# Kernel tuning notes

Measured on AMD Instinct MI355X. Metric: run time of the kernel, lower is better.

Reference implementation:

```python
import jax, jax.numpy as jnp
import numpy as np

B, N, L = 1, 2048, 256
DX, DY, H = 1536, 768, 12
D = DX // H  # head_dim = 128
EPS_MOD = 1e-6   # modulated_rmsnorm eps
EPS_QK = 1e-5    # per-head RMSNorm eps


def setup_inputs() -> dict:
    key = jax.random.key(0)
    ks = jax.random.split(key, 16)
    def n(k, shape, s=1.0):
        return jax.random.normal(k, shape, dtype=jnp.float32) * s
    # rotary tables: (N, H, D//2), shared across heads
    pos = jnp.arange(N, dtype=jnp.float32)
    inv_freq = 1.0 / (10000.0 ** (jnp.arange(D // 2, dtype=jnp.float32) / (D // 2)))
    ang = pos[:, None] * inv_freq[None, :]                       # (N, D/2)
    rope_cos = jnp.broadcast_to(jnp.cos(ang)[:, None, :], (N, H, D // 2))
    rope_sin = jnp.broadcast_to(jnp.sin(ang)[:, None, :], (N, H, D // 2))
    return {
        "x": n(ks[0], (B, N, DX)),
        "y": n(ks[1], (B, L, DY)),
        "scale_x": n(ks[2], (B, DX), 0.1),
        "scale_y": n(ks[3], (B, DY), 0.1),
        "rope_cos": rope_cos,
        "rope_sin": rope_sin,
        "Wqkv_x": n(ks[4], (DX, 3 * DX), 0.02),
        "bqkv_x": jnp.zeros((3 * DX,), jnp.float32),
        "Wqkv_y": n(ks[5], (DY, 3 * DX), 0.02),
        "bqkv_y": jnp.zeros((3 * DX,), jnp.float32),
        "q_norm_x_w": jnp.ones((D,), jnp.float32),
        "k_norm_x_w": jnp.ones((D,), jnp.float32),
        "q_norm_y_w": jnp.ones((D,), jnp.float32),
        "k_norm_y_w": jnp.ones((D,), jnp.float32),
        "Wproj_x": n(ks[6], (DX, DX), 0.02),
        "bproj_x": jnp.zeros((DX,), jnp.float32),
        "Wproj_y": n(ks[7], (DX, DY), 0.02),
        "bproj_y": jnp.zeros((DY,), jnp.float32),
    }


def _rms(v, eps):
    return v * jax.lax.rsqrt(jnp.mean(v * v, axis=-1, keepdims=True) + eps)


def _rope(q, cos, sin):
    # q: (B, S, H, D); cos/sin: (S, H, D/2); even/odd interleaved rotation
    qe, qo = q[..., 0::2], q[..., 1::2]
    re = qe * cos - qo * sin
    ro = qe * sin + qo * cos
    return jnp.stack([re, ro], axis=-1).reshape(q.shape)


def reference(x, y, scale_x, scale_y, rope_cos, rope_sin,
              Wqkv_x, bqkv_x, Wqkv_y, bqkv_y,
              q_norm_x_w, k_norm_x_w, q_norm_y_w, k_norm_y_w,
              Wproj_x, bproj_x, Wproj_y, bproj_y):
    b, n, dx = x.shape
    _, l, _ = y.shape
    h, d = H, D
    # --- visual stream ---
    xm = _rms(x, EPS_MOD) * (1.0 + scale_x[:, None, :])          # modulated_rmsnorm
    qkv = (xm @ Wqkv_x + bqkv_x).reshape(b, n, 3, h, d)
    q_x, k_x, v_x = qkv[:, :, 0], qkv[:, :, 1], qkv[:, :, 2]
    q_x = _rope(_rms(q_x, EPS_QK) * q_norm_x_w, rope_cos, rope_sin)
    k_x = _rope(_rms(k_x, EPS_QK) * k_norm_x_w, rope_cos, rope_sin)
    # --- text stream ---
    ym = _rms(y, EPS_MOD) * (1.0 + scale_y[:, None, :])
    qkvy = (ym @ Wqkv_y + bqkv_y).reshape(b, l, 3, h, d)
    q_y, k_y, v_y = qkvy[:, :, 0], qkvy[:, :, 1], qkvy[:, :, 2]
    q_y = _rms(q_y, EPS_QK) * q_norm_y_w
    k_y = _rms(k_y, EPS_QK) * k_norm_y_w
    # --- joint attention over concatenated sequence (B, H, N+L, D) ---
    q = jnp.concatenate([q_x, q_y], axis=1).transpose(0, 2, 1, 3)
    k = jnp.concatenate([k_x, k_y], axis=1).transpose(0, 2, 1, 3)
    v = jnp.concatenate([v_x, v_y], axis=1).transpose(0, 2, 1, 3)
    scale = 1.0 / np.sqrt(d).astype(np.float32)
    attn = jax.nn.softmax(jnp.einsum('bhqd,bhkd->bhqk', q, k) * scale, axis=-1)
    out = jnp.einsum('bhqk,bhkd->bhqd', attn, v)
    out = out.transpose(0, 2, 1, 3).reshape(b, n + l, h * d)
    x_out = out[:, :n] @ Wproj_x + bproj_x
    y_out = out[:, n:] @ Wproj_y + bproj_y
    return (x_out, y_out)
```

## Files before the change

### kernel.cpp

```cpp
#include <hip/hip_runtime.h>

typedef unsigned short u16;
typedef __attribute__((ext_vector_type(8))) short short8;
typedef __attribute__((ext_vector_type(4))) short short4v;
typedef __attribute__((ext_vector_type(4))) float floatx4;

__device__ __forceinline__ u16 f2bf(float f) {
  return (u16)((__float_as_uint(f) + 0x8000u) >> 16);
}
__device__ __forceinline__ float bf2f(u16 v) {
  return __uint_as_float(((unsigned)v) << 16);
}
__device__ __forceinline__ unsigned pack_bf2(float a, float b) {
  const unsigned ua = __float_as_uint(a) + 0x8000u;
  const unsigned ub = __float_as_uint(b) + 0x8000u;
  return __builtin_amdgcn_perm(ub, ua, 0x07060302);
}

#define GLD16(g, l) __builtin_amdgcn_global_load_lds( \
    (const __attribute__((address_space(1))) void*)(g), \
    (__attribute__((address_space(3))) void*)(l), 16, 0, 0)

__global__ __launch_bounds__(256) void prep(const float* __restrict__ W0, u16* __restrict__ T0,
                                            const float* __restrict__ W1, u16* __restrict__ T1,
                                            const float* __restrict__ W2, u16* __restrict__ T2,
                                            const float* __restrict__ W3, u16* __restrict__ T3,
                                            const float* __restrict__ x, const float* __restrict__ scale_x,
                                            const float* __restrict__ y, const float* __restrict__ scale_y,
                                            u16* __restrict__ xm, u16* __restrict__ ym) {
  __shared__ float t[32][33];
  const int z = blockIdx.z;
  if (z < 4) {
    const float* in; u16* out; int K, N;
    switch (z) {
      case 0: in = W0; out = T0; K = 1536; N = 4608; break;
      case 1: in = W1; out = T1; K = 768;  N = 4608; break;
      case 2: in = W2; out = T2; K = 1536; N = 1536; break;
      default: in = W3; out = T3; K = 1536; N = 768; break;
    }
    const int n0 = blockIdx.x * 32, k0 = blockIdx.y * 32;
    if (n0 >= N || k0 >= K) return;
    const int tx = threadIdx.x, ty = threadIdx.y;
#pragma unroll
    for (int i = 0; i < 32; i += 8)
      t[ty + i][tx] = in[(size_t)(k0 + ty + i) * N + n0 + tx];
    __syncthreads();
#pragma unroll
    for (int i = 0; i < 32; i += 8)
      out[(size_t)(n0 + ty + i) * K + k0 + tx] = f2bf(t[tx][ty + i]);
  } else {
    const int row = blockIdx.y * 144 + blockIdx.x;
    if (row >= 2304) return;
    const int tid = threadIdx.y * 32 + threadIdx.x;
    const float* xr; const float* sc; u16* dst; int D;
    if (row < 2048) { D = 1536; xr = x + (size_t)row * D; sc = scale_x; dst = xm + (size_t)row * D; }
    else { D = 768; xr = y + (size_t)(row - 2048) * D; sc = scale_y; dst = ym + (size_t)(row - 2048) * D; }
    float ss = 0.f;
    for (int c = tid; c < D; c += 256) { float v = xr[c]; ss += v * v; }
    for (int off = 32; off > 0; off >>= 1) ss += __shfl_down(ss, off);
    __shared__ float red[4];
    if ((tid & 63) == 0) red[tid >> 6] = ss;
    __syncthreads();
    const float tot = red[0] + red[1] + red[2] + red[3];
    const float r = rsqrtf(tot / (float)D + 1e-6f);
    for (int c = tid; c < D; c += 256)
      dst[c] = f2bf(xr[c] * r * (1.0f + sc[c]));
  }
}

template <bool BOUT>
__global__ __launch_bounds__(256) void gemm2(const u16* __restrict__ A0, const u16* __restrict__ BT0,
                                             const float* __restrict__ bias0, void* __restrict__ C0,
                                             int M0, int N0, int K0,
                                             const u16* __restrict__ A1, const u16* __restrict__ BT1,
                                             const float* __restrict__ bias1, void* __restrict__ C1,
                                             int M1, int N1, int K1) {
  const u16 *A, *BT; const float* bias; void* Cout; int M, N, K;
  if (blockIdx.z == 0) { A = A0; BT = BT0; bias = bias0; Cout = C0; M = M0; N = N0; K = K0; }
  else { A = A1; BT = BT1; bias = bias1; Cout = C1; M = M1; N = N1; K = K1; }
  const int bm = blockIdx.y * 128, bn = blockIdx.x * 128;
  if (bm >= M || bn >= N) return;

  __shared__ __align__(16) u16 As[128 * 32];
  __shared__ __align__(16) u16 Bs[128 * 32];
  const int tid = threadIdx.x;
  const int lane = tid & 63, wave = tid >> 6;
  const int wm = (wave & 1) * 64, wn = (wave >> 1) * 64;
  const int row16 = lane & 15, quad = lane >> 4;

  floatx4 acc[4][4] = {};
  const int r0 = lane >> 2, c4 = (lane & 3) * 8;
  const u16* Ag0 = A + (size_t)(bm + wave * 16 + r0) * K + c4;
  const u16* Ag1 = A + (size_t)(bm + (wave + 4) * 16 + r0) * K + c4;
  const u16* Bg0 = BT + (size_t)(bn + wave * 16 + r0) * K + c4;
  const u16* Bg1 = BT + (size_t)(bn + (wave + 4) * 16 + r0) * K + c4;
  u16* As0 = As + wave * 512; u16* As1 = As + (wave + 4) * 512;
  u16* Bs0 = Bs + wave * 512; u16* Bs1 = Bs + (wave + 4) * 512;

  for (int k0 = 0; k0 < K; k0 += 32) {
    GLD16(Ag0 + k0, As0);
    GLD16(Ag1 + k0, As1);
    GLD16(Bg0 + k0, Bs0);
    GLD16(Bg1 + k0, Bs1);
    __syncthreads();
    short8 af[4], bf[4];
#pragma unroll
    for (int i = 0; i < 4; i++) {
      af[i] = *(const short8*)&As[(wm + i * 16 + row16) * 32 + quad * 8];
      bf[i] = *(const short8*)&Bs[(wn + i * 16 + row16) * 32 + quad * 8];
    }
#pragma unroll
    for (int mi = 0; mi < 4; mi++)
#pragma unroll
      for (int ni = 0; ni < 4; ni++)
        acc[mi][ni] = __builtin_amdgcn_mfma_f32_16x16x32_bf16(af[mi], bf[ni], acc[mi][ni], 0, 0, 0);
    __syncthreads();
  }
#pragma unroll
  for (int mi = 0; mi < 4; mi++) {
#pragma unroll
    for (int ni = 0; ni < 4; ni++) {
      const int col = bn + wn + ni * 16 + row16;
      const float b = bias[col];
      const int row0 = bm + wm + mi * 16 + quad * 4;
#pragma unroll
      for (int r = 0; r < 4; r++) {
        const float v = acc[mi][ni][r] + b;
        if constexpr (BOUT)
          ((u16*)Cout)[(size_t)(row0 + r) * N + col] = f2bf(v);
        else
          ((float*)Cout)[(size_t)(row0 + r) * N + col] = v;
      }
    }
  }
}

__global__ __launch_bounds__(128) void qkv_post(const u16* __restrict__ qkvx,
                                                const u16* __restrict__ qkvy,
                                                const float* __restrict__ qnwx, const float* __restrict__ knwx,
                                                const float* __restrict__ qnwy, const float* __restrict__ knwy,
                                                const float* __restrict__ rcos, const float* __restrict__ rsin,
                                                u16* __restrict__ Q, u16* __restrict__ Kb, u16* __restrict__ V) {
  const int s = blockIdx.x, h = blockIdx.y, d = threadIdx.x;
  const bool isx = s < 2048;
  const u16* base = isx ? (qkvx + (size_t)s * 4608) : (qkvy + (size_t)(s - 2048) * 4608);
  const float q = bf2f(base[h * 128 + d]);
  const float k = bf2f(base[1536 + h * 128 + d]);
  const u16 v = base[3072 + h * 128 + d];
  __shared__ float redq[2], redk[2];
  float sq = q * q, sk = k * k;
  for (int off = 32; off > 0; off >>= 1) { sq += __shfl_down(sq, off); sk += __shfl_down(sk, off); }
  const int lane = threadIdx.x & 63, w = threadIdx.x >> 6;
  if (lane == 0) { redq[w] = sq; redk[w] = sk; }
  __syncthreads();
  const float rq = rsqrtf((redq[0] + redq[1]) * (1.f / 128.f) + 1e-5f);
  const float rk = rsqrtf((redk[0] + redk[1]) * (1.f / 128.f) + 1e-5f);
  float qn = q * rq * (isx ? qnwx[d] : qnwy[d]);
  float kn = k * rk * (isx ? knwx[d] : knwy[d]);
  if (isx) {
    const int i = d >> 1;
    const float c = rcos[((size_t)s * 12 + h) * 64 + i];
    const float sn = rsin[((size_t)s * 12 + h) * 64 + i];
    const float qo = __shfl_xor(qn, 1);
    const float ko = __shfl_xor(kn, 1);
    qn = (d & 1) ? (qo * sn + qn * c) : (qn * c - qo * sn);
    kn = (d & 1) ? (ko * sn + kn * c) : (kn * c - ko * sn);
  }
  qn *= 0.12751737942f;
  const size_t o = ((size_t)h * 2304 + s) * 128 + d;
  Q[o] = f2bf(qn);
  Kb[o] = f2bf(kn);
  V[o] = v;
}

__global__ __launch_bounds__(256) void vtrans(const u16* __restrict__ V, u16* __restrict__ Vt) {
  __shared__ u16 t[32][33];
  const int h = blockIdx.x, st = blockIdx.y * 32, dt = blockIdx.z * 32;
  const u16* Vh = V + (size_t)h * 2304 * 128;
  u16* Vth = Vt + (size_t)h * 128 * 2304;
  const int tx = threadIdx.x, ty = threadIdx.y;
#pragma unroll
  for (int i = 0; i < 32; i += 8)
    t[ty + i][tx] = Vh[(size_t)(st + ty + i) * 128 + dt + tx];
  __syncthreads();
#pragma unroll
  for (int i = 0; i < 32; i += 8)
    Vth[(size_t)(dt + ty + i) * 2304 + st + tx] = t[tx][ty + i];
}

__global__ __launch_bounds__(256, 4) void attn(const u16* __restrict__ Q, const u16* __restrict__ Kb,
                                               const u16* __restrict__ Vt,
                                               u16* __restrict__ Opart,
                                               float* __restrict__ Mp, float* __restrict__ Lp) {
  const int h = blockIdx.y, split = blockIdx.z;
  const int q0 = blockIdx.x * 64;
  const int tid = threadIdx.x, lane = tid & 63, wave = tid >> 6;
  const int row16 = lane & 15, quad = lane >> 4;
  const u16* Qh = Q + (size_t)h * 2304 * 128;
  const u16* Kh = Kb + (size_t)h * 2304 * 128;
  const u16* Vh = Vt + (size_t)h * 128 * 2304;

  __shared__ __align__(16) u16 Ks[64 * 128];
  __shared__ __align__(16) u16 Vs[128 * 64];
  __shared__ __align__(16) u16 Ps[4][16 * 64];

  short8 qf[4];
  {
    const u16* qrow = Qh + (size_t)(q0 + wave * 16 + row16) * 128;
#pragma unroll
    for (int kk = 0; kk < 4; kk++) qf[kk] = *(const short8*)(qrow + kk * 32 + quad * 8);
  }
  floatx4 oacc[8] = {};
  float m_i = -1e30f, l_i = 0.f;

  int krow[4], kcol[4], vrow[4], vcol[4];
#pragma unroll
  for (int i = 0; i < 4; i++) {
    const int j = i * 4 + wave;
    krow[i] = j * 4 + (lane >> 4);
    kcol[i] = ((lane & 15) ^ (krow[i] & 7)) * 8;
    vrow[i] = j * 8 + (lane >> 3);
    vcol[i] = ((lane & 7) ^ (vrow[i] & 7)) * 8;
  }
  const int sw = row16 & 7;
  const int kbeg = split * 576, kend = kbeg + 576;

  for (int kt = kbeg; kt < kend; kt += 64) {
    __syncthreads();
#pragma unroll
    for (int i = 0; i < 4; i++) {
      GLD16(Kh + (size_t)(kt + krow[i]) * 128 + kcol[i], Ks + (i * 4 + wave) * 512);
      GLD16(Vh + (size_t)vrow[i] * 2304 + kt + vcol[i], Vs + (i * 4 + wave) * 512);
    }
    __syncthreads();

    floatx4 sacc[4] = {};
#pragma unroll
    for (int mk = 0; mk < 4; mk++) {
#pragma unroll
      for (int kk = 0; kk < 4; kk++) {
        const int c = (4 * kk + quad) ^ sw;
        const short8 kfrag = *(const short8*)&Ks[(mk * 16 + row16) * 128 + c * 8];
        sacc[mk] = __builtin_amdgcn_mfma_f32_16x16x32_bf16(kfrag, qf[kk], sacc[mk], 0, 0, 0);
      }
    }
    float mx = sacc[0][0];
#pragma unroll
    for (int mk = 0; mk < 4; mk++)
#pragma unroll
      for (int r = 0; r < 4; r++) mx = fmaxf(mx, sacc[mk][r]);
    mx = fmaxf(mx, __shfl_xor(mx, 16));
    mx = fmaxf(mx, __shfl_xor(mx, 32));
    const float mnew = fmaxf(m_i, mx);
    if (__any(mnew > m_i)) {
      const float alpha = exp2f(m_i - mnew);
      m_i = mnew;
      const float a0 = __shfl(alpha, quad * 4 + 0);
      const float a1 = __shfl(alpha, quad * 4 + 1);
      const float a2 = __shfl(alpha, quad * 4 + 2);
      const float a3 = __shfl(alpha, quad * 4 + 3);
#pragma unroll
      for (int nd = 0; nd < 8; nd++) {
        oacc[nd][0] *= a0; oacc[nd][1] *= a1; oacc[nd][2] *= a2; oacc[nd][3] *= a3;
      }
      l_i *= alpha;
    }
    float s = 0.f;
#pragma unroll
    for (int mk = 0; mk < 4; mk++) {
#pragma unroll
      for (int r = 0; r < 4; r++) {
        const float p = exp2f(sacc[mk][r] - m_i);
        sacc[mk][r] = p;
        s += p;
      }
    }
    s += __shfl_xor(s, 16);
    s += __shfl_xor(s, 32);
    l_i += s;

#pragma unroll
    for (int mk = 0; mk < 4; mk++) {
      const int subp = (4 * mk + quad) ^ (sw << 1);
      uint2 pk;
      pk.x = pack_bf2(sacc[mk][0], sacc[mk][1]);
      pk.y = pack_bf2(sacc[mk][2], sacc[mk][3]);
      *(uint2*)&Ps[wave][row16 * 64 + subp * 4] = pk;
    }
    const int pc0 = quad ^ sw, pc1 = (4 + quad) ^ sw;
    const short8 pf0 = *(const short8*)&Ps[wave][row16 * 64 + pc0 * 8];
    const short8 pf1 = *(const short8*)&Ps[wave][row16 * 64 + pc1 * 8];
#pragma unroll
    for (int nd = 0; nd < 8; nd++) {
      const short8 vf0 = *(const short8*)&Vs[(nd * 16 + row16) * 64 + pc0 * 8];
      const short8 vf1 = *(const short8*)&Vs[(nd * 16 + row16) * 64 + pc1 * 8];
      oacc[nd] = __builtin_amdgcn_mfma_f32_16x16x32_bf16(pf0, vf0, oacc[nd], 0, 0, 0);
      oacc[nd] = __builtin_amdgcn_mfma_f32_16x16x32_bf16(pf1, vf1, oacc[nd], 0, 0, 0);
    }
  }
  const size_t base = (size_t)(split * 12 + h) * 2304 + q0 + wave * 16;
#pragma unroll
  for (int nd = 0; nd < 8; nd++)
#pragma unroll
    for (int r = 0; r < 4; r++)
      Opart[(base + quad * 4 + r) * 128 + nd * 16 + row16] = f2bf(oacc[nd][r]);
  if (lane < 16) { Mp[base + lane] = m_i; Lp[base + lane] = l_i; }
}

__global__ __launch_bounds__(256) void attn_combine(const u16* __restrict__ Opart,
                                                    const float* __restrict__ Mp,
                                                    const float* __restrict__ Lp,
                                                    u16* __restrict__ attnout) {
  const int idx = blockIdx.x * 256 + threadIdx.x;
  const int dd = (idx & 31) * 4;
  const int hq = idx >> 5;
  const int h = hq % 12, q = hq / 12;
  size_t b[4]; float ms[4], ls[4];
  float m = -1e30f;
#pragma unroll
  for (int s = 0; s < 4; s++) {
    b[s] = (size_t)(s * 12 + h) * 2304 + q;
    ms[s] = Mp[b[s]]; ls[s] = Lp[b[s]];
    m = fmaxf(m, ms[s]);
  }
  float w[4], denom = 0.f;
#pragma unroll
  for (int s = 0; s < 4; s++) { w[s] = exp2f(ms[s] - m); denom += ls[s] * w[s]; }
  const float inv = 1.0f / denom;
  float ox = 0.f, oy = 0.f, oz = 0.f, ow = 0.f;
#pragma unroll
  for (int s = 0; s < 4; s++) {
    const short4v o = *(const short4v*)&Opart[b[s] * 128 + dd];
    ox += bf2f((u16)o[0]) * w[s]; oy += bf2f((u16)o[1]) * w[s];
    oz += bf2f((u16)o[2]) * w[s]; ow += bf2f((u16)o[3]) * w[s];
  }
  short4v out;
  out[0] = (short)f2bf(ox * inv);
  out[1] = (short)f2bf(oy * inv);
  out[2] = (short)f2bf(oz * inv);
  out[3] = (short)f2bf(ow * inv);
  *(short4v*)&attnout[(size_t)idx * 4] = out;
}

extern "C" void kernel_launch(void* const* d_in, const int* in_sizes, int n_in,
                              void* d_out, int out_size, void* d_ws, size_t ws_size,
                              hipStream_t stream) {
  const float* x        = (const float*)d_in[0];
  const float* y        = (const float*)d_in[1];
  const float* scale_x  = (const float*)d_in[2];
  const float* scale_y  = (const float*)d_in[3];
  const float* rope_cos = (const float*)d_in[4];
  const float* rope_sin = (const float*)d_in[5];
  const float* Wqkv_x   = (const float*)d_in[6];
  const float* bqkv_x   = (const float*)d_in[7];
  const float* Wqkv_y   = (const float*)d_in[8];
  const float* bqkv_y   = (const float*)d_in[9];
  const float* qnwx     = (const float*)d_in[10];
  const float* knwx     = (const float*)d_in[11];
  const float* qnwy     = (const float*)d_in[12];
  const float* knwy     = (const float*)d_in[13];
  const float* Wproj_x  = (const float*)d_in[14];
  const float* bproj_x  = (const float*)d_in[15];
  const float* Wproj_y  = (const float*)d_in[16];
  const float* bproj_y  = (const float*)d_in[17];
  float* out = (float*)d_out;

  char* ws = (char*)d_ws;
  size_t off = 0;
  auto take = [&](size_t bytes) { char* p = ws + off; off += (bytes + 255) & ~(size_t)255; return p; };
  u16* WqkvxT  = (u16*)take((size_t)4608 * 1536 * 2);
  u16* WqkvyT  = (u16*)take((size_t)4608 * 768 * 2);
  u16* WprojxT = (u16*)take((size_t)1536 * 1536 * 2);
  u16* WprojyT = (u16*)take((size_t)768 * 1536 * 2);
  u16* xm      = (u16*)take((size_t)2048 * 1536 * 2);
  u16* ym      = (u16*)take((size_t)256 * 768 * 2);
  u16* qkvx    = (u16*)take((size_t)2048 * 4608 * 2);
  u16* qkvy    = (u16*)take((size_t)256 * 4608 * 2);
  u16* Qb      = (u16*)take((size_t)12 * 2304 * 128 * 2);
  u16* Kb      = (u16*)take((size_t)12 * 2304 * 128 * 2);
  u16* Vb      = (u16*)take((size_t)12 * 2304 * 128 * 2);
  u16* Vt      = (u16*)take((size_t)12 * 128 * 2304 * 2);
  u16* attnout = (u16*)take((size_t)2304 * 1536 * 2);
  u16* Opart   = (u16*)take((size_t)4 * 12 * 2304 * 128 * 2);
  float* Mp    = (float*)take((size_t)4 * 12 * 2304 * 4);
  float* Lp    = (float*)take((size_t)4 * 12 * 2304 * 4);

  prep<<<dim3(144, 48, 5), dim3(32, 8), 0, stream>>>(Wqkv_x, WqkvxT, Wqkv_y, WqkvyT,
                                                     Wproj_x, WprojxT, Wproj_y, WprojyT,
                                                     x, scale_x, y, scale_y, xm, ym);

  gemm2<true><<<dim3(36, 16, 2), 256, 0, stream>>>(xm, WqkvxT, bqkv_x, qkvx, 2048, 4608, 1536,
                                                   ym, WqkvyT, bqkv_y, qkvy, 256, 4608, 768);

  qkv_post<<<dim3(2304, 12), 128, 0, stream>>>(qkvx, qkvy, qnwx, knwx, qnwy, knwy,
                                               rope_cos, rope_sin, Qb, Kb, Vb);
  vtrans<<<dim3(12, 2304 / 32, 128 / 32), dim3(32, 8), 0, stream>>>(Vb, Vt);

  attn<<<dim3(2304 / 64, 12, 4), 256, 0, stream>>>(Qb, Kb, Vt, Opart, Mp, Lp);
  attn_combine<<<(2304 * 1536 / 4) / 256, 256, 0, stream>>>(Opart, Mp, Lp, attnout);

  gemm2<false><<<dim3(12, 16, 2), 256, 0, stream>>>(attnout, WprojxT, bproj_x, out, 2048, 1536, 1536,
                                                    attnout + (size_t)2048 * 1536, WprojyT, bproj_y,
                                                    out + (size_t)2048 * 1536, 256, 768, 1536);
  (void)in_sizes; (void)n_in; (void)out_size; (void)ws_size;
}
```

Before: 329.1 us.

## Double per-wave query rows in attention, remap blocks per XCD, lazy rescale

The attention kernel now processes 32 query rows per wave (128 per block) instead of 16, so each K/V tile loaded into LDS feeds twice as many MFMAs and global K/V traffic is halved. Blocks go on a flat 864-block grid remapped so that blocks sharing a head/split land on the same XCD, which should improve L2 reuse. The online softmax only rescales when the max grows by more than 8 (lazy rescaling), uses raw exp2 intrinsics, and packs P with v_cvt_pk_bf16_f32. The costs are higher register pressure (launch bounds lowered to 3 blocks/CU) and fewer blocks overall.

```diff
diff --git a/kernel.cpp b/kernel.cpp
--- a/kernel.cpp
+++ b/kernel.cpp
@@ -11,10 +11,10 @@
 __device__ __forceinline__ float bf2f(u16 v) {
   return __uint_as_float(((unsigned)v) << 16);
 }
-__device__ __forceinline__ unsigned pack_bf2(float a, float b) {
-  const unsigned ua = __float_as_uint(a) + 0x8000u;
-  const unsigned ub = __float_as_uint(b) + 0x8000u;
-  return __builtin_amdgcn_perm(ub, ua, 0x07060302);
+__device__ __forceinline__ unsigned cvt_pk_bf16(float a, float b) {
+  unsigned r;
+  asm("v_cvt_pk_bf16_f32 %0, %1, %2" : "=v"(r) : "v"(a), "v"(b));
+  return r;
 }
 
 #define GLD16(g, l) __builtin_amdgcn_global_load_lds( \
@@ -188,12 +188,16 @@
     Vth[(size_t)(dt + ty + i) * 2304 + st + tx] = t[tx][ty + i];
 }
 
-__global__ __launch_bounds__(256, 4) void attn(const u16* __restrict__ Q, const u16* __restrict__ Kb,
+__global__ __launch_bounds__(256, 3) void attn(const u16* __restrict__ Q, const u16* __restrict__ Kb,
                                                const u16* __restrict__ Vt,
                                                u16* __restrict__ Opart,
                                                float* __restrict__ Mp, float* __restrict__ Lp) {
-  const int h = blockIdx.y, split = blockIdx.z;
-  const int q0 = blockIdx.x * 64;
+  const int bid = blockIdx.x;
+  const int xcd = bid & 7, local = bid >> 3;
+  const int combo = xcd * 6 + local / 18;
+  const int qt = local % 18;
+  const int h = combo % 12, split = combo / 12;
+  const int q0 = qt * 128;
   const int tid = threadIdx.x, lane = tid & 63, wave = tid >> 6;
   const int row16 = lane & 15, quad = lane >> 4;
   const u16* Qh = Q + (size_t)h * 2304 * 128;
@@ -202,25 +206,28 @@
 
   __shared__ __align__(16) u16 Ks[64 * 128];
   __shared__ __align__(16) u16 Vs[128 * 64];
-  __shared__ __align__(16) u16 Ps[4][16 * 64];
-
-  short8 qf[4];
-  {
-    const u16* qrow = Qh + (size_t)(q0 + wave * 16 + row16) * 128;
-#pragma unroll
-    for (int kk = 0; kk < 4; kk++) qf[kk] = *(const short8*)(qrow + kk * 32 + quad * 8);
-  }
-  floatx4 oacc[8] = {};
-  float m_i = -1e30f, l_i = 0.f;
-
-  int krow[4], kcol[4], vrow[4], vcol[4];
+  __shared__ __align__(16) u16 Ps[4][32 * 64];
+
+  short8 qf[2][4];
+#pragma unroll
+  for (int g = 0; g < 2; g++) {
+    const u16* qrow = Qh + (size_t)(q0 + wave * 32 + g * 16 + row16) * 128;
+#pragma unroll
+    for (int kk = 0; kk < 4; kk++) qf[g][kk] = *(const short8*)(qrow + kk * 32 + quad * 8);
+  }
+  floatx4 oacc[2][8] = {};
+  float m_i[2] = {-1e30f, -1e30f}, l_i[2] = {0.f, 0.f};
+
+  const u16* Kp[4]; const u16* Vp[4];
 #pragma unroll
   for (int i = 0; i < 4; i++) {
     const int j = i * 4 + wave;
-    krow[i] = j * 4 + (lane >> 4);
-    kcol[i] = ((lane & 15) ^ (krow[i] & 7)) * 8;
-    vrow[i] = j * 8 + (lane >> 3);
-    vcol[i] = ((lane & 7) ^ (vrow[i] & 7)) * 8;
+    const int krow = j * 4 + (lane >> 4);
+    const int kcol = ((lane & 15) ^ (krow & 7)) * 8;
+    const int vrow = j * 8 + (lane >> 3);
+    const int vcol = ((lane & 7) ^ (vrow & 7)) * 8;
+    Kp[i] = Kh + (size_t)krow * 128 + kcol;
+    Vp[i] = Vh + (size_t)vrow * 2304 + vcol;
   }
   const int sw = row16 & 7;
   const int kbeg = split * 576, kend = kbeg + 576;
@@ -229,82 +236,96 @@
     __syncthreads();
 #pragma unroll
     for (int i = 0; i < 4; i++) {
-      GLD16(Kh + (size_t)(kt + krow[i]) * 128 + kcol[i], Ks + (i * 4 + wave) * 512);
-      GLD16(Vh + (size_t)vrow[i] * 2304 + kt + vcol[i], Vs + (i * 4 + wave) * 512);
-    }
-    __syncthreads();
-
-    floatx4 sacc[4] = {};
+      GLD16(Kp[i] + (size_t)kt * 128, Ks + (i * 4 + wave) * 512);
+      GLD16(Vp[i] + kt, Vs + (i * 4 + wave) * 512);
+    }
+    __syncthreads();
+
+    floatx4 sacc[2][4] = {};
 #pragma unroll
     for (int mk = 0; mk < 4; mk++) {
 #pragma unroll
       for (int kk = 0; kk < 4; kk++) {
         const int c = (4 * kk + quad) ^ sw;
         const short8 kfrag = *(const short8*)&Ks[(mk * 16 + row16) * 128 + c * 8];
-        sacc[mk] = __builtin_amdgcn_mfma_f32_16x16x32_bf16(kfrag, qf[kk], sacc[mk], 0, 0, 0);
+        sacc[0][mk] = __builtin_amdgcn_mfma_f32_16x16x32_bf16(kfrag, qf[0][kk], sacc[0][mk], 0, 0, 0);
+        sacc[1][mk] = __builtin_amdgcn_mfma_f32_16x16x32_bf16(kfrag, qf[1][kk], sacc[1][mk], 0, 0, 0);
       }
     }
-    float mx = sacc[0][0];
-#pragma unroll
-    for (int mk = 0; mk < 4; mk++)
-#pragma unroll
-      for (int r = 0; r < 4; r++) mx = fmaxf(mx, sacc[mk][r]);
-    mx = fmaxf(mx, __shfl_xor(mx, 16));
-    mx = fmaxf(mx, __shfl_xor(mx, 32));
-    const float mnew = fmaxf(m_i, mx);
-    if (__any(mnew > m_i)) {
-      const float alpha = exp2f(m_i - mnew);
-      m_i = mnew;
-      const float a0 = __shfl(alpha, quad * 4 + 0);
-      const float a1 = __shfl(alpha, quad * 4 + 1);
-      const float a2 = __shfl(alpha, quad * 4 + 2);
-      const float a3 = __shfl(alpha, quad * 4 + 3);
-#pragma unroll
-      for (int nd = 0; nd < 8; nd++) {
-        oacc[nd][0] *= a0; oacc[nd][1] *= a1; oacc[nd][2] *= a2; oacc[nd][3] *= a3;
+#pragma unroll
+    for (int g = 0; g < 2; g++) {
+      float mx = sacc[g][0][0];
+#pragma unroll
+      for (int mk = 0; mk < 4; mk++)
+#pragma unroll
+        for (int r = 0; r < 4; r++) mx = fmaxf(mx, sacc[g][mk][r]);
+      mx = fmaxf(mx, __shfl_xor(mx, 16));
+      mx = fmaxf(mx, __shfl_xor(mx, 32));
+      if (__any(mx > m_i[g] + 8.f)) {
+        const float mnew = fmaxf(m_i[g], mx);
+        const float alpha = __builtin_amdgcn_exp2f(m_i[g] - mnew);
+        m_i[g] = mnew;
+        const float a0 = __shfl(alpha, quad * 4 + 0);
+        const float a1 = __shfl(alpha, quad * 4 + 1);
+        const float a2 = __shfl(alpha, quad * 4 + 2);
+        const float a3 = __shfl(alpha, quad * 4 + 3);
+#pragma unroll
+        for (int nd = 0; nd < 8; nd++) {
+          oacc[g][nd][0] *= a0; oacc[g][nd][1] *= a1; oacc[g][nd][2] *= a2; oacc[g][nd][3] *= a3;
+        }
+        l_i[g] *= alpha;
       }
-      l_i *= alpha;
-    }
-    float s = 0.f;
-#pragma unroll
-    for (int mk = 0; mk < 4; mk++) {
-#pragma unroll
-      for (int r = 0; r < 4; r++) {
-        const float p = exp2f(sacc[mk][r] - m_i);
-        sacc[mk][r] = p;
-        s += p;
+      float s = 0.f;
+#pragma unroll
+      for (int mk = 0; mk < 4; mk++)
+#pragma unroll
+        for (int r = 0; r < 4; r++) {
+          const float p = __builtin_amdgcn_exp2f(sacc[g][mk][r] - m_i[g]);
+          sacc[g][mk][r] = p;
+          s += p;
+        }
+      s += __shfl_xor(s, 16);
+      s += __shfl_xor(s, 32);
+      l_i[g] += s;
+    }
+
+#pragma unroll
+    for (int g = 0; g < 2; g++)
+#pragma unroll
+      for (int mk = 0; mk < 4; mk++) {
+        const int subp = (4 * mk + quad) ^ (sw << 1);
+        uint2 pk;
+        pk.x = cvt_pk_bf16(sacc[g][mk][0], sacc[g][mk][1]);
+        pk.y = cvt_pk_bf16(sacc[g][mk][2], sacc[g][mk][3]);
+        *(uint2*)&Ps[wave][(g * 16 + row16) * 64 + subp * 4] = pk;
       }
-    }
-    s += __shfl_xor(s, 16);
-    s += __shfl_xor(s, 32);
-    l_i += s;
-
-#pragma unroll
-    for (int mk = 0; mk < 4; mk++) {
-      const int subp = (4 * mk + quad) ^ (sw << 1);
-      uint2 pk;
-      pk.x = pack_bf2(sacc[mk][0], sacc[mk][1]);
-      pk.y = pack_bf2(sacc[mk][2], sacc[mk][3]);
-      *(uint2*)&Ps[wave][row16 * 64 + subp * 4] = pk;
-    }
     const int pc0 = quad ^ sw, pc1 = (4 + quad) ^ sw;
-    const short8 pf0 = *(const short8*)&Ps[wave][row16 * 64 + pc0 * 8];
-    const short8 pf1 = *(const short8*)&Ps[wave][row16 * 64 + pc1 * 8];
+    short8 pf[2][2];
+#pragma unroll
+    for (int g = 0; g < 2; g++) {
+      pf[g][0] = *(const short8*)&Ps[wave][(g * 16 + row16) * 64 + pc0 * 8];
+      pf[g][1] = *(const short8*)&Ps[wave][(g * 16 + row16) * 64 + pc1 * 8];
+    }
 #pragma unroll
     for (int nd = 0; nd < 8; nd++) {
       const short8 vf0 = *(const short8*)&Vs[(nd * 16 + row16) * 64 + pc0 * 8];
       const short8 vf1 = *(const short8*)&Vs[(nd * 16 + row16) * 64 + pc1 * 8];
-      oacc[nd] = __builtin_amdgcn_mfma_f32_16x16x32_bf16(pf0, vf0, oacc[nd], 0, 0, 0);
-      oacc[nd] = __builtin_amdgcn_mfma_f32_16x16x32_bf16(pf1, vf1, oacc[nd], 0, 0, 0);
-    }
-  }
-  const size_t base = (size_t)(split * 12 + h) * 2304 + q0 + wave * 16;
-#pragma unroll
-  for (int nd = 0; nd < 8; nd++)
-#pragma unroll
-    for (int r = 0; r < 4; r++)
-      Opart[(base + quad * 4 + r) * 128 + nd * 16 + row16] = f2bf(oacc[nd][r]);
-  if (lane < 16) { Mp[base + lane] = m_i; Lp[base + lane] = l_i; }
+      oacc[0][nd] = __builtin_amdgcn_mfma_f32_16x16x32_bf16(pf[0][0], vf0, oacc[0][nd], 0, 0, 0);
+      oacc[0][nd] = __builtin_amdgcn_mfma_f32_16x16x32_bf16(pf[0][1], vf1, oacc[0][nd], 0, 0, 0);
+      oacc[1][nd] = __builtin_amdgcn_mfma_f32_16x16x32_bf16(pf[1][0], vf0, oacc[1][nd], 0, 0, 0);
+      oacc[1][nd] = __builtin_amdgcn_mfma_f32_16x16x32_bf16(pf[1][1], vf1, oacc[1][nd], 0, 0, 0);
+    }
+  }
+#pragma unroll
+  for (int g = 0; g < 2; g++) {
+    const size_t base = (size_t)(split * 12 + h) * 2304 + q0 + wave * 32 + g * 16;
+#pragma unroll
+    for (int nd = 0; nd < 8; nd++)
+#pragma unroll
+      for (int r = 0; r < 4; r++)
+        Opart[(base + quad * 4 + r) * 128 + nd * 16 + row16] = f2bf(oacc[g][nd][r]);
+    if (lane < 16) { Mp[base + lane] = m_i[g]; Lp[base + lane] = l_i[g]; }
+  }
 }
 
 __global__ __launch_bounds__(256) void attn_combine(const u16* __restrict__ Opart,
@@ -396,7 +417,7 @@
                                                rope_cos, rope_sin, Qb, Kb, Vb);
   vtrans<<<dim3(12, 2304 / 32, 128 / 32), dim3(32, 8), 0, stream>>>(Vb, Vt);
 
-  attn<<<dim3(2304 / 64, 12, 4), 256, 0, stream>>>(Qb, Kb, Vt, Opart, Mp, Lp);
+  attn<<<dim3(864), 256, 0, stream>>>(Qb, Kb, Vt, Opart, Mp, Lp);
   attn_combine<<<(2304 * 1536 / 4) / 256, 256, 0, stream>>>(Opart, Mp, Lp, attnout);
 
   gemm2<false><<<dim3(12, 16, 2), 256, 0, stream>>>(attnout, WprojxT, bproj_x, out, 2048, 1536, 1536,
```

After: 331.3 us. About the same (+0.6%).
